# Performance work log

Hardware: AMD Instinct MI355X
Metric: run time of the kernel (lower is better)

## Reference

```python
import jax, jax.numpy as jnp
import numpy as np

B, T, ENC, DEC, U = 64, 2048, 512, 512, 128

def setup_inputs() -> dict:
    key = jax.random.key(0)
    ks = jax.random.split(key, 8)
    s_dec = 1.0 / np.sqrt(DEC)
    s_enc = 1.0 / np.sqrt(ENC)
    s_u = 1.0 / np.sqrt(U)
    return {
        "decoder_hidden": jax.random.normal(ks[0], (B, DEC), jnp.float32),
        "encoder_outputs": jax.random.normal(ks[1], (B, T, ENC), jnp.float32),
        "Wa": jax.random.normal(ks[2], (DEC, U), jnp.float32) * s_dec,
        "ba": jnp.zeros((U,), jnp.float32),
        "Wb": jax.random.normal(ks[3], (ENC, U), jnp.float32) * s_enc,
        "bb": jnp.zeros((U,), jnp.float32),
        "Wv": jax.random.normal(ks[4], (U, 1), jnp.float32) * s_u,
        "bv": jnp.zeros((1,), jnp.float32),
    }

def reference(decoder_hidden, encoder_outputs, Wa, ba, Wb, bb, Wv, bv):
    # q: [B, 1, U] — decoder hidden projected, broadcast over time
    q = (decoder_hidden @ Wa + ba)[:, None, :]
    # k: [B, T, U]
    k = jnp.einsum('bte,eu->btu', encoder_outputs, Wb) + bb
    # score: [B, T, 1]
    score = jnp.tanh(q + k) @ Wv + bv
    attn = jax.nn.softmax(score, axis=1)          # [B, T, 1]
    context = jnp.sum(attn * encoder_outputs, axis=1)  # [B, ENC]
    return context, attn
```

## Files before the change

### kernel.cpp

```cpp
#include <hip/hip_runtime.h>
#include <math.h>

#define B_   64
#define T_   2048
#define ENC_ 512
#define U_   128
#define NC   16
#define MBLK 128

typedef __attribute__((ext_vector_type(8))) short short8;
typedef __attribute__((ext_vector_type(4))) float float4v;

__device__ inline unsigned short bf16_rtn(float x) {
    unsigned u = __float_as_uint(x);
    unsigned r = u + 0x7FFFu + ((u >> 16) & 1u);
    return (unsigned short)(r >> 16);
}
__device__ inline float bf16_to_f32(unsigned short h) {
    return __uint_as_float(((unsigned)h) << 16);
}

__device__ inline void cvt_split8(const float4 a0, const float4 a1,
                                  short8& h, short8& l) {
    const float xs[8] = {a0.x, a0.y, a0.z, a0.w, a1.x, a1.y, a1.z, a1.w};
#pragma unroll
    for (int j = 0; j < 8; ++j) {
        const unsigned u  = __float_as_uint(xs[j]);
        const unsigned r  = u + 0x7FFFu + ((u >> 16) & 1u);
        const unsigned hb = r >> 16;
        h[j] = (short)hb;
        const float d = xs[j] - __uint_as_float(hb << 16);
        l[j] = (short)(__float_as_uint(d) >> 16);
    }
}

__device__ inline float fast_tanh(float x) {
    const float e = __expf(2.0f * x);
    return 1.0f - 2.0f / (e + 1.0f);
}

__global__ void qproj_kernel(const float* __restrict__ dh,
                             const float* __restrict__ Wa,
                             const float* __restrict__ ba,
                             const float* __restrict__ bb,
                             float* __restrict__ q) {
    const int b = blockIdx.x;
    const int u = threadIdx.x;
    const float* dhb = dh + b * ENC_;
    float a0 = 0.f, a1 = 0.f, a2 = 0.f, a3 = 0.f;
#pragma unroll 4
    for (int e = 0; e < ENC_; e += 4) {
        a0 += dhb[e + 0] * Wa[(e + 0) * U_ + u];
        a1 += dhb[e + 1] * Wa[(e + 1) * U_ + u];
        a2 += dhb[e + 2] * Wa[(e + 2) * U_ + u];
        a3 += dhb[e + 3] * Wa[(e + 3) * U_ + u];
    }
    q[b * U_ + u] = ((a0 + a1) + (a2 + a3)) + ba[u] + bb[u];
}

__global__ void wprep_kernel(const float* __restrict__ Wb,
                             unsigned short* __restrict__ whi,
                             unsigned short* __restrict__ wlo) {
    const int fid = blockIdx.x;
    const int c   = fid >> 3;
    const int gn  = fid & 7;
    const int L   = threadIdx.x;
    const int n   = gn * 16 + (L & 15);
    const int k0  = c * 32 + (L >> 4) * 8;
    short8 hi, lo;
#pragma unroll
    for (int j = 0; j < 8; ++j) {
        const float x = Wb[(size_t)(k0 + j) * U_ + n];
        const unsigned short h = bf16_rtn(x);
        hi[j] = (short)h;
        lo[j] = (short)bf16_rtn(x - bf16_to_f32(h));
    }
    *(short8*)(whi + ((size_t)fid * 64 + L) * 8) = hi;
    *(short8*)(wlo + ((size_t)fid * 64 + L) * 8) = lo;
}

__global__ void zero_kernel(float* __restrict__ p, int n) {
    const int i = blockIdx.x * 256 + threadIdx.x;
    if (i < n) p[i] = 0.f;
}

__global__ __launch_bounds__(256)
void score_ctx_kernel(const float* __restrict__ enc,
                      const unsigned short* __restrict__ whi,
                      const unsigned short* __restrict__ wlo,
                      const float* __restrict__ q,
                      const float* __restrict__ Wv,
                      float* __restrict__ expw,
                      float* __restrict__ uctx,
                      float* __restrict__ Zsum) {
    __shared__ __align__(16) short Ahi[2][4096];
    __shared__ __align__(16) short Alo[2][4096];
    __shared__ __align__(16) short Bhi[2][4096];
    __shared__ __align__(16) short Blo[2][4096];
    __shared__ float sred[2 * MBLK];
    __shared__ float ew[MBLK];

    const int tid = threadIdx.x;
    const int w   = tid >> 6;
    const int L   = tid & 63;
    const int wr  = w >> 1;
    const int wc  = w & 1;
    const int m0  = blockIdx.x * MBLK;
    const int b   = m0 >> 11;

    const int srow = tid >> 2;
    const int sqd  = tid & 3;
    const int sf0  = ((srow >> 4) * 4 + sqd) * 16 + (srow & 15);
    const int sf1  = sf0 + 256;
    const float* encR0 = enc + (size_t)(m0 + srow) * ENC_ + sqd * 8;
    const float* encR1 = encR0 + (size_t)64 * ENC_;

    float4v acc[4][4];
#pragma unroll
    for (int mi = 0; mi < 4; ++mi)
#pragma unroll
        for (int gi = 0; gi < 4; ++gi) acc[mi][gi] = (float4v)0.f;

    {
        short8 h, l;
        cvt_split8(*(const float4*)(encR0), *(const float4*)(encR0 + 4), h, l);
        *(short8*)(&Ahi[0][sf0 * 8]) = h;
        *(short8*)(&Alo[0][sf0 * 8]) = l;
        cvt_split8(*(const float4*)(encR1), *(const float4*)(encR1 + 4), h, l);
        *(short8*)(&Ahi[0][sf1 * 8]) = h;
        *(short8*)(&Alo[0][sf1 * 8]) = l;
        *(short8*)(&Bhi[0][tid * 16])     = *(const short8*)(whi + tid * 16);
        *(short8*)(&Bhi[0][tid * 16 + 8]) = *(const short8*)(whi + tid * 16 + 8);
        *(short8*)(&Blo[0][tid * 16])     = *(const short8*)(wlo + tid * 16);
        *(short8*)(&Blo[0][tid * 16 + 8]) = *(const short8*)(wlo + tid * 16 + 8);
    }
    __syncthreads();

    for (int c = 0; c < NC; ++c) {
        const int cur = c & 1;
        float4 pa0, pa1, pa2, pa3;
        short8 pbh0, pbh1, pbl0, pbl1;
        if (c < NC - 1) {
            pa0 = *(const float4*)(encR0 + (c + 1) * 32);
            pa1 = *(const float4*)(encR0 + (c + 1) * 32 + 4);
            pa2 = *(const float4*)(encR1 + (c + 1) * 32);
            pa3 = *(const float4*)(encR1 + (c + 1) * 32 + 4);
            const unsigned short* bh = whi + (size_t)(c + 1) * 4096 + tid * 16;
            const unsigned short* bl = wlo + (size_t)(c + 1) * 4096 + tid * 16;
            pbh0 = *(const short8*)(bh);
            pbh1 = *(const short8*)(bh + 8);
            pbl0 = *(const short8*)(bl);
            pbl1 = *(const short8*)(bl + 8);
        }

        short8 ah[4], al[4], bh[4], bl[4];
#pragma unroll
        for (int mi = 0; mi < 4; ++mi) {
            const int mt = wr * 4 + mi;
            ah[mi] = *(const short8*)(&Ahi[cur][(mt * 64 + L) * 8]);
            al[mi] = *(const short8*)(&Alo[cur][(mt * 64 + L) * 8]);
        }
#pragma unroll
        for (int gi = 0; gi < 4; ++gi) {
            const int gt = wc * 4 + gi;
            bh[gi] = *(const short8*)(&Bhi[cur][(gt * 64 + L) * 8]);
            bl[gi] = *(const short8*)(&Blo[cur][(gt * 64 + L) * 8]);
        }

#pragma unroll
        for (int mi = 0; mi < 4; ++mi)
#pragma unroll
            for (int gi = 0; gi < 4; ++gi) {
                acc[mi][gi] = __builtin_amdgcn_mfma_f32_16x16x32_bf16(ah[mi], bh[gi], acc[mi][gi], 0, 0, 0);
                acc[mi][gi] = __builtin_amdgcn_mfma_f32_16x16x32_bf16(ah[mi], bl[gi], acc[mi][gi], 0, 0, 0);
                acc[mi][gi] = __builtin_amdgcn_mfma_f32_16x16x32_bf16(al[mi], bh[gi], acc[mi][gi], 0, 0, 0);
            }

        if (c < NC - 1) {
            const int nxt = cur ^ 1;
            short8 h, l;
            cvt_split8(pa0, pa1, h, l);
            *(short8*)(&Ahi[nxt][sf0 * 8]) = h;
            *(short8*)(&Alo[nxt][sf0 * 8]) = l;
            cvt_split8(pa2, pa3, h, l);
            *(short8*)(&Ahi[nxt][sf1 * 8]) = h;
            *(short8*)(&Alo[nxt][sf1 * 8]) = l;
            *(short8*)(&Bhi[nxt][tid * 16])     = pbh0;
            *(short8*)(&Bhi[nxt][tid * 16 + 8]) = pbh1;
            *(short8*)(&Blo[nxt][tid * 16])     = pbl0;
            *(short8*)(&Blo[nxt][tid * 16 + 8]) = pbl1;
        }
        __syncthreads();
    }

    const int n15 = L & 15;
    float qv[4], wvv[4];
#pragma unroll
    for (int gi = 0; gi < 4; ++gi) {
        const int u = wc * 64 + gi * 16 + n15;
        qv[gi]  = q[b * U_ + u];
        wvv[gi] = Wv[u];
    }
#pragma unroll
    for (int mi = 0; mi < 4; ++mi) {
#pragma unroll
        for (int r = 0; r < 4; ++r) {
            float s = 0.f;
#pragma unroll
            for (int gi = 0; gi < 4; ++gi)
                s += fast_tanh(qv[gi] + acc[mi][gi][r]) * wvv[gi];
            s += __shfl_xor(s, 1, 64);
            s += __shfl_xor(s, 2, 64);
            s += __shfl_xor(s, 4, 64);
            s += __shfl_xor(s, 8, 64);
            if (n15 == 0) {
                const int mrow = wr * 64 + mi * 16 + (L >> 4) * 4 + r;
                sred[wc * MBLK + mrow] = s;
            }
        }
    }
    __syncthreads();

    if (tid < MBLK) {
        const float s = sred[tid] + sred[MBLK + tid];
        const float e = __expf(s);
        ew[tid] = e;
        expw[m0 + tid] = e;
    }
    __syncthreads();

    const int col = tid * 2;
    const float* ebase = enc + (size_t)m0 * ENC_ + col;
    float sx = 0.f, sy = 0.f;
#pragma unroll 8
    for (int t = 0; t < MBLK; ++t) {
        const float wgt = ew[t];
        const float2 v = *(const float2*)(ebase + (size_t)t * ENC_);
        sx += wgt * v.x;
        sy += wgt * v.y;
    }
    atomicAdd(&uctx[b * ENC_ + col], sx);
    atomicAdd(&uctx[b * ENC_ + col + 1], sy);

    if (tid < 64) {
        float z = ew[tid] + ew[tid + 64];
        z += __shfl_xor(z, 1, 64);
        z += __shfl_xor(z, 2, 64);
        z += __shfl_xor(z, 4, 64);
        z += __shfl_xor(z, 8, 64);
        z += __shfl_xor(z, 16, 64);
        z += __shfl_xor(z, 32, 64);
        if (tid == 0) atomicAdd(&Zsum[b], z);
    }
}

__global__ void normalize_kernel(const float* __restrict__ uctx,
                                 const float* __restrict__ Zsum,
                                 const float* __restrict__ expw,
                                 float* __restrict__ ctx,
                                 float* __restrict__ attn) {
    const int idx = blockIdx.x * 256 + threadIdx.x;
    if (idx < B_ * ENC_) {
        ctx[idx] = uctx[idx] / Zsum[idx >> 9];
    } else {
        const int i2 = idx - B_ * ENC_;
        attn[i2] = expw[i2] / Zsum[i2 >> 11];
    }
}

extern "C" void kernel_launch(void* const* d_in, const int* in_sizes, int n_in,
                              void* d_out, int out_size, void* d_ws, size_t ws_size,
                              hipStream_t stream) {
    const float* dh  = (const float*)d_in[0];
    const float* enc = (const float*)d_in[1];
    const float* Wa  = (const float*)d_in[2];
    const float* ba  = (const float*)d_in[3];
    const float* Wb  = (const float*)d_in[4];
    const float* bb  = (const float*)d_in[5];
    const float* Wv  = (const float*)d_in[6];

    float* out      = (float*)d_out;
    float* ctx      = out;
    float* attn_out = out + (B_ * ENC_);

    float* ws   = (float*)d_ws;
    float* q    = ws;
    float* expw = ws + 8192;
    float* uctx = ws + 8192 + B_ * T_;
    float* Zs   = uctx + B_ * ENC_;
    unsigned short* whi = (unsigned short*)(Zs + 64);
    unsigned short* wlo = whi + 65536;

    qproj_kernel<<<B_, U_, 0, stream>>>(dh, Wa, ba, bb, q);
    wprep_kernel<<<128, 64, 0, stream>>>(Wb, whi, wlo);
    zero_kernel<<<129, 256, 0, stream>>>(uctx, B_ * ENC_ + B_);
    score_ctx_kernel<<<(B_ * T_) / MBLK, 256, 0, stream>>>(enc, whi, wlo, q, Wv,
                                                           expw, uctx, Zs);
    normalize_kernel<<<(B_ * (ENC_ + T_)) / 256, 256, 0, stream>>>(uctx, Zs, expw,
                                                                   ctx, attn_out);
}
```

Before: 433.6 us.

## Switch split GEMM to fp16 with two MFMAs and fuse prep kernels

Replaces the three-term bf16 hi/lo split GEMM with fp16, where the encoder activations are split into hi/lo fp16 pairs and the weight is kept as a single fp16 operand. This cuts the MFMA count per tile from three to two and drops the low-weight LDS buffer and its global loads. The q projection, weight conversion and zero-fill kernels are merged into one launch, and score_ctx now requests an occupancy hint of three blocks per SIMD unit. The trade-off is a narrower exponent range and a single-precision-limited weight term, which may affect accuracy.

```diff
diff --git a/kernel.cpp b/kernel.cpp
--- a/kernel.cpp
+++ b/kernel.cpp
@@ -8,29 +8,17 @@
 #define NC   16
 #define MBLK 128
 
-typedef __attribute__((ext_vector_type(8))) short short8;
+typedef __attribute__((ext_vector_type(8))) _Float16 half8;
 typedef __attribute__((ext_vector_type(4))) float float4v;
 
-__device__ inline unsigned short bf16_rtn(float x) {
-    unsigned u = __float_as_uint(x);
-    unsigned r = u + 0x7FFFu + ((u >> 16) & 1u);
-    return (unsigned short)(r >> 16);
-}
-__device__ inline float bf16_to_f32(unsigned short h) {
-    return __uint_as_float(((unsigned)h) << 16);
-}
-
-__device__ inline void cvt_split8(const float4 a0, const float4 a1,
-                                  short8& h, short8& l) {
+__device__ inline void cvt_split8_f16(const float4 a0, const float4 a1,
+                                      half8& h, half8& l) {
     const float xs[8] = {a0.x, a0.y, a0.z, a0.w, a1.x, a1.y, a1.z, a1.w};
 #pragma unroll
     for (int j = 0; j < 8; ++j) {
-        const unsigned u  = __float_as_uint(xs[j]);
-        const unsigned r  = u + 0x7FFFu + ((u >> 16) & 1u);
-        const unsigned hb = r >> 16;
-        h[j] = (short)hb;
-        const float d = xs[j] - __uint_as_float(hb << 16);
-        l[j] = (short)(__float_as_uint(d) >> 16);
+        const _Float16 hi = (_Float16)xs[j];
+        h[j] = hi;
+        l[j] = (_Float16)(xs[j] - (float)hi);
     }
 }
 
@@ -39,64 +27,60 @@
     return 1.0f - 2.0f / (e + 1.0f);
 }
 
-__global__ void qproj_kernel(const float* __restrict__ dh,
-                             const float* __restrict__ Wa,
-                             const float* __restrict__ ba,
-                             const float* __restrict__ bb,
-                             float* __restrict__ q) {
-    const int b = blockIdx.x;
-    const int u = threadIdx.x;
-    const float* dhb = dh + b * ENC_;
-    float a0 = 0.f, a1 = 0.f, a2 = 0.f, a3 = 0.f;
+__global__ __launch_bounds__(256)
+void prep_kernel(const float* __restrict__ dh,
+                 const float* __restrict__ Wa,
+                 const float* __restrict__ ba,
+                 const float* __restrict__ bb,
+                 const float* __restrict__ Wb,
+                 float* __restrict__ q,
+                 _Float16* __restrict__ whf,
+                 float* __restrict__ uz) {
+    const int blk = blockIdx.x;
+    const int tid = threadIdx.x;
+    if (blk < 64) {
+        if (tid < U_) {
+            const int b = blk, u = tid;
+            const float* dhb = dh + b * ENC_;
+            float a0 = 0.f, a1 = 0.f, a2 = 0.f, a3 = 0.f;
 #pragma unroll 4
-    for (int e = 0; e < ENC_; e += 4) {
-        a0 += dhb[e + 0] * Wa[(e + 0) * U_ + u];
-        a1 += dhb[e + 1] * Wa[(e + 1) * U_ + u];
-        a2 += dhb[e + 2] * Wa[(e + 2) * U_ + u];
-        a3 += dhb[e + 3] * Wa[(e + 3) * U_ + u];
-    }
-    q[b * U_ + u] = ((a0 + a1) + (a2 + a3)) + ba[u] + bb[u];
-}
-
-__global__ void wprep_kernel(const float* __restrict__ Wb,
-                             unsigned short* __restrict__ whi,
-                             unsigned short* __restrict__ wlo) {
-    const int fid = blockIdx.x;
-    const int c   = fid >> 3;
-    const int gn  = fid & 7;
-    const int L   = threadIdx.x;
-    const int n   = gn * 16 + (L & 15);
-    const int k0  = c * 32 + (L >> 4) * 8;
-    short8 hi, lo;
-#pragma unroll
-    for (int j = 0; j < 8; ++j) {
-        const float x = Wb[(size_t)(k0 + j) * U_ + n];
-        const unsigned short h = bf16_rtn(x);
-        hi[j] = (short)h;
-        lo[j] = (short)bf16_rtn(x - bf16_to_f32(h));
-    }
-    *(short8*)(whi + ((size_t)fid * 64 + L) * 8) = hi;
-    *(short8*)(wlo + ((size_t)fid * 64 + L) * 8) = lo;
-}
-
-__global__ void zero_kernel(float* __restrict__ p, int n) {
-    const int i = blockIdx.x * 256 + threadIdx.x;
-    if (i < n) p[i] = 0.f;
-}
-
-__global__ __launch_bounds__(256)
+            for (int e = 0; e < ENC_; e += 4) {
+                a0 += dhb[e + 0] * Wa[(e + 0) * U_ + u];
+                a1 += dhb[e + 1] * Wa[(e + 1) * U_ + u];
+                a2 += dhb[e + 2] * Wa[(e + 2) * U_ + u];
+                a3 += dhb[e + 3] * Wa[(e + 3) * U_ + u];
+            }
+            q[b * U_ + u] = ((a0 + a1) + (a2 + a3)) + ba[u] + bb[u];
+        }
+    } else if (blk < 96) {
+        const int fid = (blk - 64) * 4 + (tid >> 6);
+        const int c   = fid >> 3;
+        const int gn  = fid & 7;
+        const int L   = tid & 63;
+        const int n   = gn * 16 + (L & 15);
+        const int k0  = c * 32 + (L >> 4) * 8;
+        half8 hi;
+#pragma unroll
+        for (int j = 0; j < 8; ++j)
+            hi[j] = (_Float16)Wb[(size_t)(k0 + j) * U_ + n];
+        *(half8*)(whf + ((size_t)fid * 64 + L) * 8) = hi;
+    } else {
+        const int i = (blk - 96) * 256 + tid;
+        if (i < B_ * ENC_ + B_) uz[i] = 0.f;
+    }
+}
+
+__global__ __launch_bounds__(256, 3)
 void score_ctx_kernel(const float* __restrict__ enc,
-                      const unsigned short* __restrict__ whi,
-                      const unsigned short* __restrict__ wlo,
+                      const _Float16* __restrict__ whf,
                       const float* __restrict__ q,
                       const float* __restrict__ Wv,
                       float* __restrict__ expw,
                       float* __restrict__ uctx,
                       float* __restrict__ Zsum) {
-    __shared__ __align__(16) short Ahi[2][4096];
-    __shared__ __align__(16) short Alo[2][4096];
-    __shared__ __align__(16) short Bhi[2][4096];
-    __shared__ __align__(16) short Blo[2][4096];
+    __shared__ __align__(16) _Float16 Ahi[2][4096];
+    __shared__ __align__(16) _Float16 Alo[2][4096];
+    __shared__ __align__(16) _Float16 Bh[2][4096];
     __shared__ float sred[2 * MBLK];
     __shared__ float ew[MBLK];
 
@@ -122,73 +106,64 @@
         for (int gi = 0; gi < 4; ++gi) acc[mi][gi] = (float4v)0.f;
 
     {
-        short8 h, l;
-        cvt_split8(*(const float4*)(encR0), *(const float4*)(encR0 + 4), h, l);
-        *(short8*)(&Ahi[0][sf0 * 8]) = h;
-        *(short8*)(&Alo[0][sf0 * 8]) = l;
-        cvt_split8(*(const float4*)(encR1), *(const float4*)(encR1 + 4), h, l);
-        *(short8*)(&Ahi[0][sf1 * 8]) = h;
-        *(short8*)(&Alo[0][sf1 * 8]) = l;
-        *(short8*)(&Bhi[0][tid * 16])     = *(const short8*)(whi + tid * 16);
-        *(short8*)(&Bhi[0][tid * 16 + 8]) = *(const short8*)(whi + tid * 16 + 8);
-        *(short8*)(&Blo[0][tid * 16])     = *(const short8*)(wlo + tid * 16);
-        *(short8*)(&Blo[0][tid * 16 + 8]) = *(const short8*)(wlo + tid * 16 + 8);
+        half8 h, l;
+        cvt_split8_f16(*(const float4*)(encR0), *(const float4*)(encR0 + 4), h, l);
+        *(half8*)(&Ahi[0][sf0 * 8]) = h;
+        *(half8*)(&Alo[0][sf0 * 8]) = l;
+        cvt_split8_f16(*(const float4*)(encR1), *(const float4*)(encR1 + 4), h, l);
+        *(half8*)(&Ahi[0][sf1 * 8]) = h;
+        *(half8*)(&Alo[0][sf1 * 8]) = l;
+        *(half8*)(&Bh[0][tid * 16])     = *(const half8*)(whf + tid * 16);
+        *(half8*)(&Bh[0][tid * 16 + 8]) = *(const half8*)(whf + tid * 16 + 8);
     }
     __syncthreads();
 
     for (int c = 0; c < NC; ++c) {
         const int cur = c & 1;
         float4 pa0, pa1, pa2, pa3;
-        short8 pbh0, pbh1, pbl0, pbl1;
+        half8 pb0, pb1;
         if (c < NC - 1) {
             pa0 = *(const float4*)(encR0 + (c + 1) * 32);
             pa1 = *(const float4*)(encR0 + (c + 1) * 32 + 4);
             pa2 = *(const float4*)(encR1 + (c + 1) * 32);
             pa3 = *(const float4*)(encR1 + (c + 1) * 32 + 4);
-            const unsigned short* bh = whi + (size_t)(c + 1) * 4096 + tid * 16;
-            const unsigned short* bl = wlo + (size_t)(c + 1) * 4096 + tid * 16;
-            pbh0 = *(const short8*)(bh);
-            pbh1 = *(const short8*)(bh + 8);
-            pbl0 = *(const short8*)(bl);
-            pbl1 = *(const short8*)(bl + 8);
-        }
-
-        short8 ah[4], al[4], bh[4], bl[4];
+            const _Float16* bp = whf + (size_t)(c + 1) * 4096 + tid * 16;
+            pb0 = *(const half8*)(bp);
+            pb1 = *(const half8*)(bp + 8);
+        }
+
+        half8 ah[4], al[4], bh[4];
 #pragma unroll
         for (int mi = 0; mi < 4; ++mi) {
             const int mt = wr * 4 + mi;
-            ah[mi] = *(const short8*)(&Ahi[cur][(mt * 64 + L) * 8]);
-            al[mi] = *(const short8*)(&Alo[cur][(mt * 64 + L) * 8]);
+            ah[mi] = *(const half8*)(&Ahi[cur][(mt * 64 + L) * 8]);
+            al[mi] = *(const half8*)(&Alo[cur][(mt * 64 + L) * 8]);
         }
 #pragma unroll
         for (int gi = 0; gi < 4; ++gi) {
             const int gt = wc * 4 + gi;
-            bh[gi] = *(const short8*)(&Bhi[cur][(gt * 64 + L) * 8]);
-            bl[gi] = *(const short8*)(&Blo[cur][(gt * 64 + L) * 8]);
+            bh[gi] = *(const half8*)(&Bh[cur][(gt * 64 + L) * 8]);
         }
 
 #pragma unroll
         for (int mi = 0; mi < 4; ++mi)
 #pragma unroll
             for (int gi = 0; gi < 4; ++gi) {
-                acc[mi][gi] = __builtin_amdgcn_mfma_f32_16x16x32_bf16(ah[mi], bh[gi], acc[mi][gi], 0, 0, 0);
-                acc[mi][gi] = __builtin_amdgcn_mfma_f32_16x16x32_bf16(ah[mi], bl[gi], acc[mi][gi], 0, 0, 0);
-                acc[mi][gi] = __builtin_amdgcn_mfma_f32_16x16x32_bf16(al[mi], bh[gi], acc[mi][gi], 0, 0, 0);
+                acc[mi][gi] = __builtin_amdgcn_mfma_f32_16x16x32_f16(ah[mi], bh[gi], acc[mi][gi], 0, 0, 0);
+                acc[mi][gi] = __builtin_amdgcn_mfma_f32_16x16x32_f16(al[mi], bh[gi], acc[mi][gi], 0, 0, 0);
             }
 
         if (c < NC - 1) {
             const int nxt = cur ^ 1;
-            short8 h, l;
-            cvt_split8(pa0, pa1, h, l);
-            *(short8*)(&Ahi[nxt][sf0 * 8]) = h;
-            *(short8*)(&Alo[nxt][sf0 * 8]) = l;
-            cvt_split8(pa2, pa3, h, l);
-            *(short8*)(&Ahi[nxt][sf1 * 8]) = h;
-            *(short8*)(&Alo[nxt][sf1 * 8]) = l;
-            *(short8*)(&Bhi[nxt][tid * 16])     = pbh0;
-            *(short8*)(&Bhi[nxt][tid * 16 + 8]) = pbh1;
-            *(short8*)(&Blo[nxt][tid * 16])     = pbl0;
-            *(short8*)(&Blo[nxt][tid * 16 + 8]) = pbl1;
+            half8 h, l;
+            cvt_split8_f16(pa0, pa1, h, l);
+            *(half8*)(&Ahi[nxt][sf0 * 8]) = h;
+            *(half8*)(&Alo[nxt][sf0 * 8]) = l;
+            cvt_split8_f16(pa2, pa3, h, l);
+            *(half8*)(&Ahi[nxt][sf1 * 8]) = h;
+            *(half8*)(&Alo[nxt][sf1 * 8]) = l;
+            *(half8*)(&Bh[nxt][tid * 16])     = pb0;
+            *(half8*)(&Bh[nxt][tid * 16 + 8]) = pb1;
         }
         __syncthreads();
     }
@@ -288,13 +263,10 @@
     float* expw = ws + 8192;
     float* uctx = ws + 8192 + B_ * T_;
     float* Zs   = uctx + B_ * ENC_;
-    unsigned short* whi = (unsigned short*)(Zs + 64);
-    unsigned short* wlo = whi + 65536;
-
-    qproj_kernel<<<B_, U_, 0, stream>>>(dh, Wa, ba, bb, q);
-    wprep_kernel<<<128, 64, 0, stream>>>(Wb, whi, wlo);
-    zero_kernel<<<129, 256, 0, stream>>>(uctx, B_ * ENC_ + B_);
-    score_ctx_kernel<<<(B_ * T_) / MBLK, 256, 0, stream>>>(enc, whi, wlo, q, Wv,
+    _Float16* whf = (_Float16*)(Zs + 64);
+
+    prep_kernel<<<225, 256, 0, stream>>>(dh, Wa, ba, bb, Wb, q, whf, uctx);
+    score_ctx_kernel<<<(B_ * T_) / MBLK, 256, 0, stream>>>(enc, whf, q, Wv,
                                                            expw, uctx, Zs);
     normalize_kernel<<<(B_ * (ENC_ + T_)) / 256, 256, 0, stream>>>(uctx, Zs, expw,
                                                                    ctx, attn_out);
```

After: 432.2 us. Within noise of the previous version (-0.3%).
